# Optimization experiments

Hardware: AMD Instinct MI355X
Metric: run time of the kernel (lower is better)

## Reference

```python
import jax, jax.numpy as jnp
import numpy as np
import math

B = 32
TS_LEN = 8192
DSEG = 32
S = TS_LEN // DSEG          # 256 segments
DM = 256                    # dim_model
NBITS = 8                   # bits of the bucket signature (synthetic _compute_index)
NBUCKETS = 2 ** NBITS       # 256 ragged-vocab buckets, made uniform here
W = 512                     # words per bucket (uniform -> vocabulary_dist[b] = b*W)
NHAAR = 6                   # min(log2(S)=8, max_haar_depth=6)
LMAX = 13                   # full haar depth of wavedec on length-8192 signal


def _layer_norm(x, eps=1e-5):
    m = x.mean(-1, keepdims=True)
    v = ((x - m) ** 2).mean(-1, keepdims=True)
    return (x - m) / jnp.sqrt(v + eps)


def _pos_emb():
    # sinusoidal positional embedding, matches the torch buffer construction
    pos = jnp.arange(S, dtype=jnp.float32)[:, None]
    div = jnp.exp(jnp.arange(0, DM, 2, dtype=jnp.float32) * (-math.log(10000.0) / DM))
    pe = jnp.zeros((S, DM), jnp.float32)
    pe = pe.at[:, 0::2].set(jnp.sin(pos * div))
    pe = pe.at[:, 1::2].set(jnp.cos(pos * div))
    return pe


def setup_inputs() -> dict:
    key = jax.random.key(0)
    k1, k2, k3, k4 = jax.random.split(key, 4)
    x = jax.random.normal(k1, (B, TS_LEN), jnp.float32)
    # candidate words live in [0,1] (they are compared against min-max-normalized segments)
    vocab_table = jax.random.uniform(k2, (NBUCKETS, W, DSEG), dtype=jnp.float32)
    word_emb = jax.random.normal(k3, (NBUCKETS * W, DM), jnp.float32)
    haar_emb = jax.random.normal(k4, (NHAAR + 1, DM), jnp.float32)
    return {"x": x, "vocab_table": vocab_table, "word_emb": word_emb, "haar_emb": haar_emb}


def reference(x, vocab_table, word_emb, haar_emb):
    # ---- _adjust: input length == ts_len -> identity, att_mask all ones ----
    att_mask = jnp.ones((B, S), jnp.int32)

    # ---- compute_word_embedding (vectorized over batch and segments) ----
    segs = x.reshape(B, S, DSEG)
    smin = segs.min(-1, keepdims=True)
    smax = segs.max(-1, keepdims=True)
    seg_norm = (segs - smin) / (smax - smin + 1e-8)
    # synthetic _compute_index: 8-bit signature (chunk mean above segment mean)
    chunk_means = segs.reshape(B, S, NBITS, DSEG // NBITS).mean(-1)       # [B,S,8]
    bits = (chunk_means > segs.mean(-1, keepdims=True)).astype(jnp.int32)
    bucket = (bits * (2 ** jnp.arange(NBITS, dtype=jnp.int32))).sum(-1)   # [B,S]
    cand = vocab_table[bucket]                                            # [B,S,W,DSEG]
    dist = jnp.abs(cand - seg_norm[:, :, None, :]).sum(-1)                # [B,S,W] L1 cdist
    best = jnp.argmin(dist, axis=-1)                                      # [B,S]
    word_embed = word_emb[bucket * W + best]                              # [B,S,DM]

    # ---- compute_haar_embedding (pywt.wavedec with 'haar', first NHAAR+1 coeffs) ----
    a = x
    details = []
    sqrt2 = jnp.float32(math.sqrt(2.0))
    for _ in range(LMAX):
        even = a[:, 0::2]
        odd = a[:, 1::2]
        details.append((even - odd) / sqrt2)
        a = (even + odd) / sqrt2
    coeffs = [a] + details[::-1]                # [cA_L, cD_L, ..., cD_1]
    taken = coeffs[: NHAAR + 1]
    rows = [jnp.repeat(c, S // c.shape[1], axis=1) for c in taken]        # each [B,S]
    haar_matrix = jnp.stack(rows, axis=-1)                                # [B,S,NHAAR+1]
    haar_matrix = haar_matrix * att_mask[..., None].astype(haar_matrix.dtype)
    haar_embed = haar_matrix @ haar_emb                                   # [B,S,DM]
    haar_embed = _layer_norm(haar_embed)

    out = word_embed + haar_embed + _pos_emb()
    out = _layer_norm(out)
    return (out, att_mask)
```

## Files before the change

### kernel.cpp

```cpp
#include <hip/hip_runtime.h>
#include <math.h>

#define BB 32
#define TS 8192
#define DSEG 32
#define SS 256
#define DM 256
#define W 512
#define CAP 1024

__global__ __launch_bounds__(64) void haar_kernel(const float* __restrict__ x,
                                                  float* __restrict__ hout) {
    const int b = blockIdx.x;
    const int lane = threadIdx.x;
    const float* xb = x + (size_t)b * TS + (size_t)lane * 128;

    float a[128];
#pragma unroll
    for (int i = 0; i < 32; ++i) {
        float4 u = *(const float4*)(xb + 4 * i);
        a[4 * i + 0] = u.x; a[4 * i + 1] = u.y;
        a[4 * i + 2] = u.z; a[4 * i + 3] = u.w;
    }
    const float is2 = 0.70710678118654752440f;
#pragma unroll
    for (int len = 128; len > 1; len >>= 1) {
#pragma unroll
        for (int j = 0; j < (len >> 1); ++j)
            a[j] = (a[2 * j] + a[2 * j + 1]) * is2;
    }
    float val = a[0];
    float* ob = hout + b * 64;
#pragma unroll
    for (int len = 64; len > 1; len >>= 1) {
        float e = __shfl(val, 2 * lane);
        float o = __shfl(val, 2 * lane + 1);
        int half = len >> 1;
        if (lane < half) {
            ob[half + lane] = (e - o) * is2;
            val = (e + o) * is2;
        }
    }
    if (lane == 0) ob[0] = val;
}

__global__ __launch_bounds__(256) void prep_kernel(
    const float* __restrict__ x,
    float* __restrict__ segn_g,
    unsigned char* __restrict__ bucketc,
    unsigned long long* __restrict__ bestkey)
{
    const int t = threadIdx.x;
    const int segBase = blockIdx.x * 8;
    __shared__ float sseg[8][32];
    sseg[t >> 5][t & 31] = x[(size_t)segBase * 32 + t];
    __syncthreads();

    const int hw = t >> 5;
    const int h = hw & 1;
    const int l = t & 31;
    const int seg = segBase + hw;

    float v = sseg[hw][l];
    float mn = v, mx = v, sm = v;
#pragma unroll
    for (int m = 1; m <= 16; m <<= 1) {
        mn = fminf(mn, __shfl_xor(mn, m));
        mx = fmaxf(mx, __shfl_xor(mx, m));
        sm += __shfl_xor(sm, m);
    }
    float mean = sm * (1.0f / 32.0f);
    float cm = 0.0f;
    if (l < 8) {
        cm = ((sseg[hw][4 * l] + sseg[hw][4 * l + 1]) + sseg[hw][4 * l + 2]) +
             sseg[hw][4 * l + 3];
        cm *= 0.25f;
    }
    unsigned long long bal = __ballot(l < 8 && cm > mean);
    segn_g[(size_t)seg * 32 + l] = (v - mn) / (mx - mn + 1e-8f);
    if (l == 0) bucketc[seg] = (unsigned char)((bal >> (h * 32)) & 0xFF);
    if (l == 1) bestkey[seg] = ~0ULL;
}

__global__ __launch_bounds__(512) void search_kernel(
    const float* __restrict__ vocab,
    const float* __restrict__ segn_g,
    const unsigned char* __restrict__ bucketc,
    unsigned long long* __restrict__ bestkey)
{
    const int bucket = blockIdx.x >> 1;
    const int half = blockIdx.x & 1;
    const int t = threadIdx.x;
    const int lane = t & 63;
    const int wid = t >> 6;

    __shared__ float vsh[256 * 32];
    __shared__ int list[CAP];
    __shared__ int cnt;
    if (t == 0) cnt = 0;
    __syncthreads();

    for (int i = t; i < BB * SS; i += 512) {
        if (bucketc[i] == (unsigned char)bucket) {
            int p = atomicAdd(&cnt, 1);
            if (p < CAP) list[p] = i;
        }
    }

    const float* vb = vocab + ((size_t)bucket * W + (size_t)half * 256) * DSEG;
#pragma unroll 2
    for (int f = t; f < 2048; f += 512) {
        int r = f >> 3, q = f & 7;
        float4 u = ((const float4*)vb)[f];
        int sq = q ^ (r & 7);
        *(float4*)&vsh[r * 32 + sq * 4] = u;
    }
    __syncthreads();

    int n = cnt; if (n > CAP) n = CAP;
    for (int i = wid; i < n; i += 8) {
        const int seg = list[i];
        const float* sp = segn_g + (size_t)seg * 32;
        float sv[32];
#pragma unroll
        for (int d = 0; d < 32; ++d) sv[d] = sp[d];

        unsigned long long best = ~0ULL;
#pragma unroll
        for (int c = 0; c < 4; ++c) {
            const int r = c * 64 + lane;
            float dist = 0.0f;
#pragma unroll
            for (int q = 0; q < 8; ++q) {
                float4 u = *(const float4*)&vsh[r * 32 + ((q ^ (r & 7)) * 4)];
                dist += fabsf(u.x - sv[4 * q + 0]);
                dist += fabsf(u.y - sv[4 * q + 1]);
                dist += fabsf(u.z - sv[4 * q + 2]);
                dist += fabsf(u.w - sv[4 * q + 3]);
            }
            unsigned w = (unsigned)(half * 256 + r);
            unsigned long long key =
                ((unsigned long long)__float_as_uint(dist) << 32) | w;
            if (key < best) best = key;
        }
#pragma unroll
        for (int m = 1; m < 64; m <<= 1) {
            unsigned long long o = __shfl_xor(best, m);
            if (o < best) best = o;
        }
        if (lane == 0) atomicMin(bestkey + seg, best);
    }
}

__global__ __launch_bounds__(256) void out_kernel(
    const float* __restrict__ wemb,
    const float* __restrict__ hemb,
    const float* __restrict__ hcoef,
    const unsigned char* __restrict__ bucketc,
    const unsigned long long* __restrict__ bestkey,
    float* __restrict__ out)
{
    const int bs = blockIdx.x;
    const int b = bs >> 8;
    const int s = bs & 255;
    const int t = threadIdx.x;
    const int lane = t & 63;
    const int wid = t >> 6;

    __shared__ float rA[4], rB[4];

    const int bucket = bucketc[bs];
    const int bestw = (int)(unsigned)(bestkey[bs] & 0xFFFFFFFFull);

    const float* hb = hcoef + b * 64;
    float hk[7];
    hk[0] = hb[0];
#pragma unroll
    for (int k = 1; k <= 6; ++k)
        hk[k] = hb[(1 << (k - 1)) + (s >> (8 - (k - 1)))];

    float h = 0.0f;
#pragma unroll
    for (int k = 0; k < 7; ++k) h += hk[k] * hemb[k * DM + t];

    float sm = h, sq = h * h;
#pragma unroll
    for (int m = 1; m < 64; m <<= 1) {
        sm += __shfl_xor(sm, m);
        sq += __shfl_xor(sq, m);
    }
    if (lane == 0) { rA[wid] = sm; rB[wid] = sq; }
    __syncthreads();
    sm = ((rA[0] + rA[1]) + rA[2]) + rA[3];
    sq = ((rB[0] + rB[1]) + rB[2]) + rB[3];
    float mh = sm * (1.0f / 256.0f);
    float vh = fmaxf(sq * (1.0f / 256.0f) - mh * mh, 0.0f);
    float hn = (h - mh) / sqrtf(vh + 1e-5f);

    const size_t row = (size_t)bucket * W + (size_t)bestw;
    float wv = wemb[row * DM + t];

    const float cexp = -9.210340371976184f / 256.0f;
    float dv = expf((float)(t & ~1) * cexp);
    float ang = (float)s * dv;
    float pe = (t & 1) ? cosf(ang) : sinf(ang);

    float o = wv + hn + pe;

    __syncthreads();
    float sm2 = o, sq2 = o * o;
#pragma unroll
    for (int m = 1; m < 64; m <<= 1) {
        sm2 += __shfl_xor(sm2, m);
        sq2 += __shfl_xor(sq2, m);
    }
    if (lane == 0) { rA[wid] = sm2; rB[wid] = sq2; }
    __syncthreads();
    sm2 = ((rA[0] + rA[1]) + rA[2]) + rA[3];
    sq2 = ((rB[0] + rB[1]) + rB[2]) + rB[3];
    float mo = sm2 * (1.0f / 256.0f);
    float vo = fmaxf(sq2 * (1.0f / 256.0f) - mo * mo, 0.0f);
    float on = (o - mo) / sqrtf(vo + 1e-5f);

    out[(size_t)bs * DM + t] = on;
    if (t == 0) out[(size_t)BB * SS * DM + bs] = 1.0f;
}

extern "C" void kernel_launch(void* const* d_in, const int* in_sizes, int n_in,
                              void* d_out, int out_size, void* d_ws, size_t ws_size,
                              hipStream_t stream) {
    const float* x     = (const float*)d_in[0];
    const float* vocab = (const float*)d_in[1];
    const float* wemb  = (const float*)d_in[2];
    const float* hemb  = (const float*)d_in[3];
    float* out = (float*)d_out;

    char* ws = (char*)d_ws;
    float* segn                  = (float*)ws;
    unsigned long long* bestkey  = (unsigned long long*)(ws + 1048576);
    unsigned char* bucketc       = (unsigned char*)(ws + 1048576 + 65536);
    float* hco                   = (float*)(ws + 1048576 + 65536 + 8192);

    prep_kernel<<<1024, 256, 0, stream>>>(x, segn, bucketc, bestkey);
    haar_kernel<<<BB, 64, 0, stream>>>(x, hco);
    search_kernel<<<512, 512, 0, stream>>>(vocab, segn, bucketc, bestkey);
    out_kernel<<<BB * SS, 256, 0, stream>>>(wemb, hemb, hco, bucketc, bestkey, out);
}
```

Before: 222.6 us.

## Merge haar into prep kernel and make output layernorm one wave per row

The haar kernel is folded into the prep kernel as 32 extra blocks, which removes one launch. The haar first level is now applied while loading, so the register array is halved. The output kernel now handles one row per 64-lane wave using float4 loads and stores, so the shared-memory reductions and block barriers go away. Each lane computes four elements and evaluates fewer exp calls for the positional encoding.

```diff
diff --git a/kernel.cpp b/kernel.cpp
--- a/kernel.cpp
+++ b/kernel.cpp
@@ -9,77 +9,80 @@
 #define W 512
 #define CAP 1024
 
-__global__ __launch_bounds__(64) void haar_kernel(const float* __restrict__ x,
-                                                  float* __restrict__ hout) {
-    const int b = blockIdx.x;
-    const int lane = threadIdx.x;
-    const float* xb = x + (size_t)b * TS + (size_t)lane * 128;
-
-    float a[128];
-#pragma unroll
-    for (int i = 0; i < 32; ++i) {
-        float4 u = *(const float4*)(xb + 4 * i);
-        a[4 * i + 0] = u.x; a[4 * i + 1] = u.y;
-        a[4 * i + 2] = u.z; a[4 * i + 3] = u.w;
-    }
-    const float is2 = 0.70710678118654752440f;
-#pragma unroll
-    for (int len = 128; len > 1; len >>= 1) {
-#pragma unroll
-        for (int j = 0; j < (len >> 1); ++j)
-            a[j] = (a[2 * j] + a[2 * j + 1]) * is2;
-    }
-    float val = a[0];
-    float* ob = hout + b * 64;
-#pragma unroll
-    for (int len = 64; len > 1; len >>= 1) {
-        float e = __shfl(val, 2 * lane);
-        float o = __shfl(val, 2 * lane + 1);
-        int half = len >> 1;
-        if (lane < half) {
-            ob[half + lane] = (e - o) * is2;
-            val = (e + o) * is2;
-        }
-    }
-    if (lane == 0) ob[0] = val;
-}
-
-__global__ __launch_bounds__(256) void prep_kernel(
+__global__ __launch_bounds__(256) void prep_haar_kernel(
     const float* __restrict__ x,
     float* __restrict__ segn_g,
     unsigned char* __restrict__ bucketc,
-    unsigned long long* __restrict__ bestkey)
+    unsigned long long* __restrict__ bestkey,
+    float* __restrict__ hout)
 {
+    const int blk = blockIdx.x;
     const int t = threadIdx.x;
-    const int segBase = blockIdx.x * 8;
-    __shared__ float sseg[8][32];
-    sseg[t >> 5][t & 31] = x[(size_t)segBase * 32 + t];
-    __syncthreads();
-
-    const int hw = t >> 5;
-    const int h = hw & 1;
-    const int l = t & 31;
-    const int seg = segBase + hw;
-
-    float v = sseg[hw][l];
-    float mn = v, mx = v, sm = v;
-#pragma unroll
-    for (int m = 1; m <= 16; m <<= 1) {
-        mn = fminf(mn, __shfl_xor(mn, m));
-        mx = fmaxf(mx, __shfl_xor(mx, m));
-        sm += __shfl_xor(sm, m);
-    }
-    float mean = sm * (1.0f / 32.0f);
-    float cm = 0.0f;
-    if (l < 8) {
-        cm = ((sseg[hw][4 * l] + sseg[hw][4 * l + 1]) + sseg[hw][4 * l + 2]) +
-             sseg[hw][4 * l + 3];
-        cm *= 0.25f;
-    }
-    unsigned long long bal = __ballot(l < 8 && cm > mean);
-    segn_g[(size_t)seg * 32 + l] = (v - mn) / (mx - mn + 1e-8f);
-    if (l == 0) bucketc[seg] = (unsigned char)((bal >> (h * 32)) & 0xFF);
-    if (l == 1) bestkey[seg] = ~0ULL;
+
+    if (blk < 1024) {
+        const int segBase = blk * 8;
+        __shared__ float sseg[8][32];
+        sseg[t >> 5][t & 31] = x[(size_t)segBase * 32 + t];
+        __syncthreads();
+
+        const int hw = t >> 5;
+        const int h = hw & 1;
+        const int l = t & 31;
+        const int seg = segBase + hw;
+
+        float v = sseg[hw][l];
+        float mn = v, mx = v, sm = v;
+#pragma unroll
+        for (int m = 1; m <= 16; m <<= 1) {
+            mn = fminf(mn, __shfl_xor(mn, m));
+            mx = fmaxf(mx, __shfl_xor(mx, m));
+            sm += __shfl_xor(sm, m);
+        }
+        float mean = sm * (1.0f / 32.0f);
+        float cm = 0.0f;
+        if (l < 8) {
+            cm = ((sseg[hw][4 * l] + sseg[hw][4 * l + 1]) + sseg[hw][4 * l + 2]) +
+                 sseg[hw][4 * l + 3];
+            cm *= 0.25f;
+        }
+        unsigned long long bal = __ballot(l < 8 && cm > mean);
+        segn_g[(size_t)seg * 32 + l] = (v - mn) / (mx - mn + 1e-8f);
+        if (l == 0) bucketc[seg] = (unsigned char)((bal >> (h * 32)) & 0xFF);
+        if (l == 1) bestkey[seg] = ~0ULL;
+    } else {
+        const int b = blk - 1024;
+        const int lane = t;
+        if (lane >= 64) return;
+        const float* xb = x + (size_t)b * TS + (size_t)lane * 128;
+        const float is2 = 0.70710678118654752440f;
+
+        float a[64];
+#pragma unroll
+        for (int i = 0; i < 32; ++i) {
+            float4 u = *(const float4*)(xb + 4 * i);
+            a[2 * i + 0] = (u.x + u.y) * is2;
+            a[2 * i + 1] = (u.z + u.w) * is2;
+        }
+#pragma unroll
+        for (int len = 64; len > 1; len >>= 1) {
+#pragma unroll
+            for (int j = 0; j < (len >> 1); ++j)
+                a[j] = (a[2 * j] + a[2 * j + 1]) * is2;
+        }
+        float val = a[0];
+        float* ob = hout + b * 64;
+#pragma unroll
+        for (int len = 64; len > 1; len >>= 1) {
+            float e = __shfl(val, 2 * lane);
+            float o = __shfl(val, 2 * lane + 1);
+            int half = len >> 1;
+            if (lane < half) {
+                ob[half + lane] = (e - o) * is2;
+                val = (e + o) * is2;
+            }
+        }
+        if (lane == 0) ob[0] = val;
+    }
 }
 
 __global__ __launch_bounds__(512) void search_kernel(
@@ -160,14 +163,10 @@
     const unsigned long long* __restrict__ bestkey,
     float* __restrict__ out)
 {
-    const int bs = blockIdx.x;
+    const int bs = (blockIdx.x << 2) + (threadIdx.x >> 6);
+    const int lane = threadIdx.x & 63;
     const int b = bs >> 8;
     const int s = bs & 255;
-    const int t = threadIdx.x;
-    const int lane = t & 63;
-    const int wid = t >> 6;
-
-    __shared__ float rA[4], rB[4];
 
     const int bucket = bucketc[bs];
     const int bestw = (int)(unsigned)(bestkey[bs] & 0xFFFFFFFFull);
@@ -179,51 +178,55 @@
     for (int k = 1; k <= 6; ++k)
         hk[k] = hb[(1 << (k - 1)) + (s >> (8 - (k - 1)))];
 
-    float h = 0.0f;
-#pragma unroll
-    for (int k = 0; k < 7; ++k) h += hk[k] * hemb[k * DM + t];
-
-    float sm = h, sq = h * h;
+    float h0 = 0.f, h1 = 0.f, h2 = 0.f, h3 = 0.f;
+#pragma unroll
+    for (int k = 0; k < 7; ++k) {
+        float4 he = ((const float4*)(hemb + k * DM))[lane];
+        h0 += hk[k] * he.x; h1 += hk[k] * he.y;
+        h2 += hk[k] * he.z; h3 += hk[k] * he.w;
+    }
+
+    float sm = ((h0 + h1) + h2) + h3;
+    float sq = ((h0 * h0 + h1 * h1) + h2 * h2) + h3 * h3;
 #pragma unroll
     for (int m = 1; m < 64; m <<= 1) {
         sm += __shfl_xor(sm, m);
         sq += __shfl_xor(sq, m);
     }
-    if (lane == 0) { rA[wid] = sm; rB[wid] = sq; }
-    __syncthreads();
-    sm = ((rA[0] + rA[1]) + rA[2]) + rA[3];
-    sq = ((rB[0] + rB[1]) + rB[2]) + rB[3];
     float mh = sm * (1.0f / 256.0f);
     float vh = fmaxf(sq * (1.0f / 256.0f) - mh * mh, 0.0f);
-    float hn = (h - mh) / sqrtf(vh + 1e-5f);
+    float rs = 1.0f / sqrtf(vh + 1e-5f);
+    float n0 = (h0 - mh) * rs, n1 = (h1 - mh) * rs;
+    float n2 = (h2 - mh) * rs, n3 = (h3 - mh) * rs;
 
     const size_t row = (size_t)bucket * W + (size_t)bestw;
-    float wv = wemb[row * DM + t];
+    float4 wv = ((const float4*)(wemb + row * DM))[lane];
 
     const float cexp = -9.210340371976184f / 256.0f;
-    float dv = expf((float)(t & ~1) * cexp);
-    float ang = (float)s * dv;
-    float pe = (t & 1) ? cosf(ang) : sinf(ang);
-
-    float o = wv + hn + pe;
-
-    __syncthreads();
-    float sm2 = o, sq2 = o * o;
+    float dva = expf((float)(4 * lane) * cexp);
+    float dvb = expf((float)(4 * lane + 2) * cexp);
+    float anga = (float)s * dva, angb = (float)s * dvb;
+    float o0 = wv.x + n0 + sinf(anga);
+    float o1 = wv.y + n1 + cosf(anga);
+    float o2 = wv.z + n2 + sinf(angb);
+    float o3 = wv.w + n3 + cosf(angb);
+
+    float sm2 = ((o0 + o1) + o2) + o3;
+    float sq2 = ((o0 * o0 + o1 * o1) + o2 * o2) + o3 * o3;
 #pragma unroll
     for (int m = 1; m < 64; m <<= 1) {
         sm2 += __shfl_xor(sm2, m);
         sq2 += __shfl_xor(sq2, m);
     }
-    if (lane == 0) { rA[wid] = sm2; rB[wid] = sq2; }
-    __syncthreads();
-    sm2 = ((rA[0] + rA[1]) + rA[2]) + rA[3];
-    sq2 = ((rB[0] + rB[1]) + rB[2]) + rB[3];
     float mo = sm2 * (1.0f / 256.0f);
     float vo = fmaxf(sq2 * (1.0f / 256.0f) - mo * mo, 0.0f);
-    float on = (o - mo) / sqrtf(vo + 1e-5f);
-
-    out[(size_t)bs * DM + t] = on;
-    if (t == 0) out[(size_t)BB * SS * DM + bs] = 1.0f;
+    float rs2 = 1.0f / sqrtf(vo + 1e-5f);
+
+    float4 res;
+    res.x = (o0 - mo) * rs2; res.y = (o1 - mo) * rs2;
+    res.z = (o2 - mo) * rs2; res.w = (o3 - mo) * rs2;
+    ((float4*)(out + (size_t)bs * DM))[lane] = res;
+    if (lane == 0) out[(size_t)BB * SS * DM + bs] = 1.0f;
 }
 
 extern "C" void kernel_launch(void* const* d_in, const int* in_sizes, int n_in,
@@ -241,8 +244,7 @@
     unsigned char* bucketc       = (unsigned char*)(ws + 1048576 + 65536);
     float* hco                   = (float*)(ws + 1048576 + 65536 + 8192);
 
-    prep_kernel<<<1024, 256, 0, stream>>>(x, segn, bucketc, bestkey);
-    haar_kernel<<<BB, 64, 0, stream>>>(x, hco);
+    prep_haar_kernel<<<1056, 256, 0, stream>>>(x, segn, bucketc, bestkey, hco);
     search_kernel<<<512, 512, 0, stream>>>(vocab, segn, bucketc, bestkey);
-    out_kernel<<<BB * SS, 256, 0, stream>>>(wemb, hemb, hco, bucketc, bestkey, out);
-}
+    out_kernel<<<2048, 256, 0, stream>>>(wemb, hemb, hco, bucketc, bestkey, out);
+}
```

After: 214.6 us. 1.04x faster.
